# Kernel optimization log

Measured on AMD Instinct MI355X. Metric: run time of the kernel, lower is better.

## Reference

```python
import jax, jax.numpy as jnp
import numpy as np

B, L, D = 16, 2048, 192  # batch, frames_per_data, units
H, K = 4, 12             # num_heads, key_dim (hardcoded in build())
EPS = 1e-3               # keras LayerNormalization default epsilon


def layer_norm(x, g, b):
    m = jnp.mean(x, axis=-1, keepdims=True)
    v = jnp.mean(jnp.square(x - m), axis=-1, keepdims=True)
    return (x - m) * jax.lax.rsqrt(v + EPS) * g + b


def conv1d_valid(x, w, b):
    # x: [B,L,C], w: [3,Cin,Cout] -> [B,L-2,Cout]
    return jax.lax.conv_general_dilated(
        x, w, window_strides=(1,), padding='VALID',
        dimension_numbers=('NWC', 'WIO', 'NWC')) + b


def setup_inputs() -> dict:
    key = jax.random.key(0)
    ks = jax.random.split(key, 16)
    s = 0.05
    return {
        'x': jax.random.normal(ks[0], (B, L, D), jnp.float32),
        'ln1_g': jnp.ones((D,), jnp.float32),
        'ln1_b': jnp.zeros((D,), jnp.float32),
        'wq': jax.random.normal(ks[1], (D, H, K), jnp.float32) * s,
        'bq': jnp.zeros((H, K), jnp.float32),
        'wk': jax.random.normal(ks[2], (D, H, K), jnp.float32) * s,
        'bk': jnp.zeros((H, K), jnp.float32),
        'wv': jax.random.normal(ks[3], (D, H, K), jnp.float32) * s,
        'bv': jnp.zeros((H, K), jnp.float32),
        'wo': jax.random.normal(ks[4], (H, K, D), jnp.float32) * s,
        'bo': jnp.zeros((D,), jnp.float32),
        'ln2_g': jnp.ones((D,), jnp.float32),
        'ln2_b': jnp.zeros((D,), jnp.float32),
        'c1_w': jax.random.normal(ks[5], (3, D, D), jnp.float32) * s,
        'c1_b': jnp.zeros((D,), jnp.float32),
        'c2_w': jax.random.normal(ks[6], (3, D, D), jnp.float32) * s,
        'c2_b': jnp.zeros((D,), jnp.float32),
    }


def reference(x, ln1_g, ln1_b, wq, bq, wk, bk, wv, bv, wo, bo,
              ln2_g, ln2_b, c1_w, c1_b, c2_w, c2_b):
    # --- LN1 + causal MHA + residual (dropout = identity at inference) ---
    xn = layer_norm(x, ln1_g, ln1_b)
    q = jnp.einsum('bld,dhk->blhk', xn, wq) + bq
    k = jnp.einsum('bld,dhk->blhk', xn, wk) + bk
    v = jnp.einsum('bld,dhk->blhk', xn, wv) + bv
    scores = jnp.einsum('blhk,bmhk->bhlm', q, k) / jnp.sqrt(jnp.float32(K))
    causal = jnp.tril(jnp.ones((L, L), jnp.float32))  # tril(True) mask
    scores = scores + (1.0 - causal) * (-1e9)          # keras additive mask
    attn = jax.nn.softmax(scores, axis=-1)
    ctx = jnp.einsum('bhlm,bmhk->blhk', attn, v)
    mha = jnp.einsum('blhk,hkd->bld', ctx, wo) + bo
    x = x + mha
    # --- LN2 + positionwise Conv1D feedforward + residual ---
    xn = layer_norm(x, ln2_g, ln2_b)
    h = jax.nn.relu(conv1d_valid(xn, c1_w, c1_b))      # [B,L-2,D]
    h = jnp.pad(h, ((0, 0), (1, 1), (0, 0)))           # ZeroPadding1D(1,1)
    h = conv1d_valid(h, c2_w, c2_b)                    # [B,L-2,D]
    h = jnp.pad(h, ((0, 0), (1, 1), (0, 0)))
    return x + h
```

## Files before the change

### kernel.cpp

```cpp
#include <hip/hip_runtime.h>
#include <hip/hip_bf16.h>

#define L_ 2048
#define D_ 192
#define HK_ 48
#define EPS_ 1e-3f
#define SCALE_ 0.28867513459481287f
#define LOG2E_ 1.4426950408889634f

typedef __hip_bfloat16 bf16;
typedef _Float16 f16;
typedef __fp16 hf16x2 __attribute__((ext_vector_type(2)));
typedef _Float16 f16x4 __attribute__((ext_vector_type(4)));
typedef __bf16 bf16x4 __attribute__((ext_vector_type(4)));
typedef __bf16 bf16x8 __attribute__((ext_vector_type(8)));
typedef float  f32x4  __attribute__((ext_vector_type(4)));

__device__ __forceinline__ float b2f(bf16 x) { return __bfloat162float(x); }
__device__ __forceinline__ bf16 f2b(float x) { return __float2bfloat16(x); }

__global__ __launch_bounds__(256) void k_prep_all(
    const float* __restrict__ c1w, const float* __restrict__ c2w,
    const float* __restrict__ wq, const float* __restrict__ wk, const float* __restrict__ wv,
    const float* __restrict__ bq, const float* __restrict__ bk, const float* __restrict__ bv,
    const float* __restrict__ wo,
    bf16* __restrict__ wrep1, bf16* __restrict__ wrep2,
    bf16* __restrict__ wrepq, float* __restrict__ bias144, bf16* __restrict__ wrepo)
{
    const int i = blockIdx.x * 256 + threadIdx.x;
    if (i < 110592) {
        const int k = i / 192, n = i - k * 192;
        wrep1[((size_t)(k >> 5) * 192 + n) * 32 + (k & 31)] = f2b(c1w[i]);
    } else if (i < 221184) {
        const int j = i - 110592;
        const int k = j / 192, n = j - k * 192;
        wrep2[((size_t)(k >> 5) * 192 + n) * 32 + (k & 31)] = f2b(c2w[j]);
    } else if (i < 248832) {
        const int j = i - 221184;
        const int kb = j / 4608, rem = j % 4608;
        const int n = rem / 32, kk = rem % 32;
        const int k = kb * 32 + kk;
        float v;
        if (n < 48)       v = wq[k * HK_ + n] * (SCALE_ * LOG2E_);
        else if (n < 96)  v = wk[k * HK_ + (n - 48)];
        else              v = wv[k * HK_ + (n - 96)];
        wrepq[j] = f2b(v);
    } else if (i < 248976) {
        const int j = i - 248832;
        bias144[j] = (j < 48) ? bq[j] * (SCALE_ * LOG2E_)
                   : (j < 96) ? bk[j - 48] : bv[j - 96];
    } else if (i < 261264) {
        const int j = i - 248976;
        const int kb = j / 6144, rem = j % 6144;
        const int n = rem / 32, kk = rem % 32;
        const int k = kb * 32 + kk;
        wrepo[j] = f2b(k < 48 ? wo[k * D_ + n] : 0.f);
    }
}

__global__ __launch_bounds__(256, 4) void k_ln_qkv(
    const float* __restrict__ x, const float* __restrict__ g1, const float* __restrict__ b1,
    const bf16* __restrict__ wrep, const float* __restrict__ bias144,
    f16* __restrict__ qo, f16* __restrict__ ko, f16* __restrict__ vt)
{
    __shared__ bf16 xn[32 * 200];
    const int tid = threadIdx.x;
    const int wave = tid >> 6, lane = tid & 63;
    const int rowbase = blockIdx.x * 32;
    const int b = rowbase >> 11;
    const int lrow0 = rowbase & 2047;

    const float gg0 = g1[lane], gg1 = g1[lane + 64], gg2 = g1[lane + 128];
    const float bb0 = b1[lane], bb1 = b1[lane + 64], bb2 = b1[lane + 128];
    for (int i = 0; i < 8; ++i) {
        const int r = wave * 8 + i;
        const float* xp = x + (size_t)(rowbase + r) * D_;
        const float x0 = xp[lane];
        const float x1 = xp[lane + 64];
        const float x2 = xp[lane + 128];
        float s = x0 + x1 + x2;
        float q = x0 * x0 + x1 * x1 + x2 * x2;
        #pragma unroll
        for (int m = 1; m < 64; m <<= 1) {
            s += __shfl_xor(s, m, 64);
            q += __shfl_xor(q, m, 64);
        }
        const float mean = s * (1.0f / 192.0f);
        const float var  = q * (1.0f / 192.0f) - mean * mean;
        const float rs   = rsqrtf(var + EPS_);
        xn[r * 200 + lane]       = f2b((x0 - mean) * rs * gg0 + bb0);
        xn[r * 200 + lane + 64]  = f2b((x1 - mean) * rs * gg1 + bb1);
        xn[r * 200 + lane + 128] = f2b((x2 - mean) * rs * gg2 + bb2);
    }

    if (tid < 128) {
        const int h  = tid >> 5;
        const int vc = 12 + ((tid >> 3) & 3);
        const int p0 = lrow0 + (tid & 7) * 4;
        f16x4 vv;
        vv[0] = vv[1] = vv[2] = vv[3] = (vc == 12) ? (f16)1.0f : (f16)0.0f;
        *(f16x4*)(vt + ((size_t)(b * 4 + h) * 16 + vc) * 2048 + p0) = vv;
    }
    __syncthreads();

    const int l15 = lane & 15, q4 = lane >> 4;
    const int rt = wave >> 1, g = wave & 1;
    const int ntlim = 5 - g;
    f32x4 acc[5];
    #pragma unroll
    for (int nt = 0; nt < 5; ++nt) acc[nt] = (f32x4){0.f, 0.f, 0.f, 0.f};

    const bf16* xrow = xn + (rt * 16 + l15) * 200 + q4 * 8;
    #pragma unroll
    for (int kb = 0; kb < 6; ++kb) {
        const bf16x8 a = *(const bf16x8*)(xrow + kb * 32);
        const bf16* wp = wrep + ((size_t)kb * 144 + l15) * 32 + q4 * 8
                       + (size_t)(g * 5) * 16 * 32;
        #pragma unroll
        for (int nt = 0; nt < 5; ++nt) {
            if (nt < ntlim) {
                const bf16x8 bfr = *(const bf16x8*)(wp + (size_t)nt * 16 * 32);
                acc[nt] = __builtin_amdgcn_mfma_f32_16x16x32_bf16(a, bfr, acc[nt], 0, 0, 0);
            }
        }
    }

    const int lr0 = lrow0 + rt * 16 + q4 * 4;
    #pragma unroll
    for (int nt = 0; nt < 5; ++nt) {
        if (nt < ntlim) {
            const int ntg = g * 5 + nt;
            const int col = ntg * 16 + l15;
            const float bd = bias144[col];
            if (ntg < 3) {
                const int h2 = col / 12, c12 = col - h2 * 12;
                #pragma unroll
                for (int reg = 0; reg < 4; ++reg)
                    qo[((size_t)(b * 4 + h2) * 2048 + lr0 + reg) * 12 + c12] =
                        (f16)(acc[nt][reg] + bd);
            } else if (ntg < 6) {
                const int ck = col - 48;
                const int h2 = ck / 12, c12 = ck - h2 * 12;
                #pragma unroll
                for (int reg = 0; reg < 4; ++reg)
                    ko[((size_t)(b * 4 + h2) * 2048 + lr0 + reg) * 12 + c12] =
                        (f16)(acc[nt][reg] + bd);
            } else {
                const int vcol = col - 96;
                const int h = vcol / 12, c12 = vcol % 12;
                f16x4 vv;
                #pragma unroll
                for (int reg = 0; reg < 4; ++reg) vv[reg] = (f16)(acc[nt][reg] + bd);
                *(f16x4*)(vt + ((size_t)(b * 4 + h) * 16 + c12) * 2048 +
                          lrow0 + rt * 16 + q4 * 4) = vv;
            }
        }
    }
}

__global__ __launch_bounds__(256, 8) void k_attn(
    const f16* __restrict__ qh, const f16* __restrict__ kh, const f16* __restrict__ vt,
    bf16* __restrict__ ctx)
{
    const int tid = threadIdx.x;
    const int wv = tid >> 6, lane = tid & 63;
    const int quad = lane >> 4, l15 = lane & 15;
    const int bh = blockIdx.x & 63;
    const int qtile = 15 - (blockIdx.x >> 6);
    const int b = bh >> 2, h = bh & 3;
    const size_t base  = (size_t)bh * 2048 * 12;
    const size_t vbase = ((size_t)bh * 16 + l15) * 2048;
    const int qw = qtile * 128 + wv * 32;
    const int q16 = qw >> 4;
    const int ntot = q16 + 2;

    f16x4 Qf[2];
    #pragma unroll
    for (int s = 0; s < 2; ++s) {
        f16x4 v;
        if (quad < 3)
            v = *(const f16x4*)(qh + base + (size_t)(qw + s * 16 + l15) * 12 + quad * 4);
        else { v[0] = (f16)LOG2E_; v[1] = 0; v[2] = 0; v[3] = 0; }
        Qf[s] = v;
    }

    f32x4 O[2];
    O[0] = (f32x4){0.f, 0.f, 0.f, 0.f};
    O[1] = (f32x4){0.f, 0.f, 0.f, 0.f};

    f16x4 Kg[2], Vg[2];
    #pragma unroll
    for (int u = 0; u < 2; ++u) {
        if (quad < 3)
            Kg[u] = *(const f16x4*)(kh + base + (size_t)(u * 16 + l15) * 12 + quad * 4);
        else { Kg[u][0] = (f16)-6.0f; Kg[u][1] = 0; Kg[u][2] = 0; Kg[u][3] = 0; }
        Vg[u] = *(const f16x4*)(vt + vbase + u * 16 + quad * 4);
    }

    for (int t = 0; t < ntot; t += 2) {
        f16x4 Kn[2], Vn[2];
        if (t + 2 < ntot) {
            #pragma unroll
            for (int u = 0; u < 2; ++u) {
                const int kt = t + 2 + u;
                if (quad < 3)
                    Kn[u] = *(const f16x4*)(kh + base + (size_t)(kt * 16 + l15) * 12 + quad * 4);
                else { Kn[u][0] = (f16)-6.0f; Kn[u][1] = 0; Kn[u][2] = 0; Kn[u][3] = 0; }
                Vn[u] = *(const f16x4*)(vt + vbase + kt * 16 + quad * 4);
            }
        }
        const bool masked = (t >= q16);
        #pragma unroll
        for (int u = 0; u < 2; ++u) {
            const int k0 = (t + u) * 16 + quad * 4;
            #pragma unroll
            for (int s = 0; s < 2; ++s) {
                f32x4 sc = (f32x4){0.f, 0.f, 0.f, 0.f};
                sc = __builtin_amdgcn_mfma_f32_16x16x16f16(Kg[u], Qf[s], sc, 0, 0, 0);
                float p0 = __builtin_amdgcn_exp2f(sc[0]);
                float p1 = __builtin_amdgcn_exp2f(sc[1]);
                float p2 = __builtin_amdgcn_exp2f(sc[2]);
                float p3 = __builtin_amdgcn_exp2f(sc[3]);
                if (masked) {
                    const int qg = qw + s * 16 + l15;
                    p0 = (k0 + 0 <= qg) ? p0 : 0.f;
                    p1 = (k0 + 1 <= qg) ? p1 : 0.f;
                    p2 = (k0 + 2 <= qg) ? p2 : 0.f;
                    p3 = (k0 + 3 <= qg) ? p3 : 0.f;
                }
                const hf16x2 lo = __builtin_amdgcn_cvt_pkrtz(p0, p1);
                const hf16x2 hi = __builtin_amdgcn_cvt_pkrtz(p2, p3);
                f16x4 p;
                p[0] = (f16)lo[0]; p[1] = (f16)lo[1];
                p[2] = (f16)hi[0]; p[3] = (f16)hi[1];
                O[s] = __builtin_amdgcn_mfma_f32_16x16x16f16(p, Vg[u], O[s], 0, 0, 0);
            }
        }
        Kg[0] = Kn[0]; Kg[1] = Kn[1];
        Vg[0] = Vn[0]; Vg[1] = Vn[1];
    }

    const int src = (quad << 4) + 12;
    #pragma unroll
    for (int s = 0; s < 2; ++s) {
        #pragma unroll
        for (int j = 0; j < 4; ++j) {
            const float li  = __shfl(O[s][j], src, 64);
            const float inv = __builtin_amdgcn_rcpf(li);
            if (l15 < 12)
                ctx[(size_t)(b * 2048 + qw + s * 16 + quad * 4 + j) * 48 + h * 12 + l15]
                    = f2b(O[s][j] * inv);
        }
    }
}

__global__ __launch_bounds__(256, 4) void k_proj_ln2(
    const float* __restrict__ x, const bf16* __restrict__ ctx,
    const bf16* __restrict__ wrepo,
    const float* __restrict__ bo, const float* __restrict__ g2,
    const float* __restrict__ lb2, bf16* __restrict__ x2b,
    bf16* __restrict__ xn2b)
{
    __shared__ bf16 ct[32 * 72];
    __shared__ float psum[4][4][4][2];
    const int tid = threadIdx.x;
    const int wave = tid >> 6, lane = tid & 63;
    const int rowbase = blockIdx.x * 32;

    {
        const int row6 = tid / 6, c6 = tid - row6 * 6;
        if (tid < 192) {
            const bf16x8 v = *(const bf16x8*)(ctx + (size_t)(rowbase + row6) * 48 + c6 * 8);
            *(bf16x8*)(ct + row6 * 72 + c6 * 8) = v;
        }
        const int rz = tid / 3, cz = tid - rz * 3;
        if (tid < 96) {
            bf16x8 z;
            #pragma unroll
            for (int i = 0; i < 8; ++i) z[i] = (__bf16)0.0f;
            *(bf16x8*)(ct + rz * 72 + 48 + cz * 8) = z;
        }
    }
    __syncthreads();

    const int l15 = lane & 15, q4 = lane >> 4;
    const int rt = wave >> 1, g = wave & 1;
    f32x4 acc[6];
    #pragma unroll
    for (int j = 0; j < 6; ++j) acc[j] = (f32x4){0.f, 0.f, 0.f, 0.f};
    const bf16* arow = ct + (rt * 16 + l15) * 72 + q4 * 8;
    #pragma unroll
    for (int kb = 0; kb < 2; ++kb) {
        const bf16x8 a = *(const bf16x8*)(arow + kb * 32);
        const bf16* wp = wrepo + ((size_t)kb * 192 + l15) * 32 + q4 * 8
                       + (size_t)(g * 6) * 16 * 32;
        #pragma unroll
        for (int j = 0; j < 6; ++j) {
            const bf16x8 bb = *(const bf16x8*)(wp + (size_t)j * 16 * 32);
            acc[j] = __builtin_amdgcn_mfma_f32_16x16x32_bf16(a, bb, acc[j], 0, 0, 0);
        }
    }

    const int rw0 = rowbase + rt * 16 + q4 * 4;
    float sum[4] = {0.f, 0.f, 0.f, 0.f}, ssum[4] = {0.f, 0.f, 0.f, 0.f};
    #pragma unroll
    for (int j = 0; j < 6; ++j) {
        const int col = (g * 6 + j) * 16 + l15;
        const float bod = bo[col];
        #pragma unroll
        for (int reg = 0; reg < 4; ++reg) {
            const float v = acc[j][reg] + bod + x[(size_t)(rw0 + reg) * D_ + col];
            acc[j][reg] = v;
            x2b[(size_t)(rw0 + reg) * D_ + col] = f2b(v);
            sum[reg] += v; ssum[reg] += v * v;
        }
    }
    #pragma unroll
    for (int m = 1; m <= 8; m <<= 1) {
        #pragma unroll
        for (int reg = 0; reg < 4; ++reg) {
            sum[reg]  += __shfl_xor(sum[reg], m, 64);
            ssum[reg] += __shfl_xor(ssum[reg], m, 64);
        }
    }
    if (l15 == 0) {
        #pragma unroll
        for (int reg = 0; reg < 4; ++reg) {
            psum[wave][q4][reg][0] = sum[reg];
            psum[wave][q4][reg][1] = ssum[reg];
        }
    }
    __syncthreads();
    float mean[4], rs[4];
    #pragma unroll
    for (int reg = 0; reg < 4; ++reg) {
        const float st  = sum[reg]  + psum[wave ^ 1][q4][reg][0];
        const float qt2 = ssum[reg] + psum[wave ^ 1][q4][reg][1];
        mean[reg] = st * (1.0f / 192.0f);
        const float var = qt2 * (1.0f / 192.0f) - mean[reg] * mean[reg];
        rs[reg] = rsqrtf(var + EPS_);
    }
    #pragma unroll
    for (int j = 0; j < 6; ++j) {
        const int col = (g * 6 + j) * 16 + l15;
        const float gg = g2[col], bb2 = lb2[col];
        #pragma unroll
        for (int reg = 0; reg < 4; ++reg)
            xn2b[(size_t)(rw0 + reg) * D_ + col] =
                f2b((acc[j][reg] - mean[reg]) * rs[reg] * gg + bb2);
    }
}

#define INROWB 416
#define NIN    36
#define NH     34
#define HTOFF  (NIN * INROWB)
__global__ __launch_bounds__(256, 4) void k_conv_fused(
    const bf16* __restrict__ act, const bf16* __restrict__ w1,
    const float* __restrict__ b1c, const bf16* __restrict__ w2,
    const float* __restrict__ b2c, const bf16* __restrict__ x2b,
    float* __restrict__ outf)
{
    __shared__ __align__(16) char lds[NIN * INROWB + NH * INROWB];

    const int tid = threadIdx.x;
    const int wave = tid >> 6, lane = tid & 63;
    const int m16 = lane & 15, q = lane >> 4;
    const int rowbase = blockIdx.x * 32;
    const int lrow = rowbase & (L_ - 1);

    {
        const bf16* src0 = act + ((long long)rowbase - 2) * D_;
        bf16x8 v[4];
        int dst[4];
        #pragma unroll
        for (int i = 0; i < 4; ++i) {
            const int g = tid + i * 256;
            if (g < 864) {
                v[i] = *(const bf16x8*)(src0 + g * 8);
                const int row = (g * 2731) >> 16;
                dst[i] = row * INROWB + (g - row * 24) * 16;
            }
        }
        #pragma unroll
        for (int i = 0; i < 4; ++i) {
            const int g = tid + i * 256;
            if (g < 864) *(bf16x8*)(lds + dst[i]) = v[i];
        }
    }

    const int laneA = m16 * INROWB + q * 16;
    const int colw = wave * 48;
    float bd1[3], bd2[3];
    #pragma unroll
    for (int j = 0; j < 3; ++j) {
        bd1[j] = b1c[colw + j * 16 + m16];
        bd2[j] = b2c[colw + j * 16 + m16];
    }
    __syncthreads();

    f32x4 acc1[3][3];
    #pragma unroll
    for (int mt = 0; mt < 3; ++mt)
        #pragma unroll
        for (int j = 0; j < 3; ++j) acc1[mt][j] = (f32x4){0.f, 0.f, 0.f, 0.f};

    #define LOADB(w, kb, j) \
        (*(const bf16x8*)((w) + ((size_t)(kb) * 192 + m16) * 32 + q * 8 \
                          + (size_t)(wave * 3 + (j)) * 16 * 32))
    {
        bf16x8 bB[2][3];
        #pragma unroll
        for (int j = 0; j < 3; ++j) bB[0][j] = LOADB(w1, 0, j);
        #pragma unroll
        for (int kb = 0; kb < 18; ++kb) {
            if (kb + 1 < 18) {
                #pragma unroll
                for (int j = 0; j < 3; ++j) bB[(kb + 1) & 1][j] = LOADB(w1, kb + 1, j);
            }
            const int t = kb / 6, c6 = kb % 6;
            bf16x8 a[3];
            #pragma unroll
            for (int mt = 0; mt < 3; ++mt)
                a[mt] = *(const bf16x8*)(lds + laneA + (mt * 16 + t) * INROWB + c6 * 64);
            #pragma unroll
            for (int j = 0; j < 3; ++j)
                #pragma unroll
                for (int mt = 0; mt < 3; ++mt)
                    acc1[mt][j] = __builtin_amdgcn_mfma_f32_16x16x32_bf16(
                        a[mt], bB[kb & 1][j], acc1[mt][j], 0, 0, 0);
        }
    }

    #pragma unroll
    for (int mt = 0; mt < 3; ++mt)
        #pragma unroll
        for (int j = 0; j < 3; ++j)
            #pragma unroll
            for (int reg = 0; reg < 4; ++reg) {
                const int hr = mt * 16 + q * 4 + reg;
                if (hr < NH) {
                    const int hm = lrow + hr - 1;
                    float v = fmaxf(acc1[mt][j][reg] + bd1[j], 0.f);
                    if (hm == 0 || hm == L_ - 1) v = 0.f;
                    *(bf16*)(lds + HTOFF + hr * INROWB + (colw + j * 16 + m16) * 2) = f2b(v);
                }
            }

    float xr[3][2][4];
    #pragma unroll
    for (int j = 0; j < 3; ++j)
        #pragma unroll
        for (int mt = 0; mt < 2; ++mt)
            #pragma unroll
            for (int reg = 0; reg < 4; ++reg)
                xr[j][mt][reg] = b2f(x2b[(size_t)(rowbase + mt * 16 + q * 4 + reg) * D_
                                         + colw + j * 16 + m16]);
    __syncthreads();

    f32x4 acc2[2][3];
    #pragma unroll
    for (int mt = 0; mt < 2; ++mt)
        #pragma unroll
        for (int j = 0; j < 3; ++j) acc2[mt][j] = (f32x4){0.f, 0.f, 0.f, 0.f};
    {
        bf16x8 bB[2][3];
        #pragma unroll
        for (int j = 0; j < 3; ++j) bB[0][j] = LOADB(w2, 0, j);
        #pragma unroll
        for (int kb = 0; kb < 18; ++kb) {
            if (kb + 1 < 18) {
                #pragma unroll
                for (int j = 0; j < 3; ++j) bB[(kb + 1) & 1][j] = LOADB(w2, kb + 1, j);
            }
            const int t = kb / 6, c6 = kb % 6;
            bf16x8 a[2];
            #pragma unroll
            for (int mt = 0; mt < 2; ++mt)
                a[mt] = *(const bf16x8*)(lds + HTOFF + laneA + (mt * 16 + t) * INROWB + c6 * 64);
            #pragma unroll
            for (int j = 0; j < 3; ++j)
                #pragma unroll
                for (int mt = 0; mt < 2; ++mt)
                    acc2[mt][j] = __builtin_amdgcn_mfma_f32_16x16x32_bf16(
                        a[mt], bB[kb & 1][j], acc2[mt][j], 0, 0, 0);
        }
    }
    #undef LOADB

    #pragma unroll
    for (int j = 0; j < 3; ++j)
        #pragma unroll
        for (int mt = 0; mt < 2; ++mt)
            #pragma unroll
            for (int reg = 0; reg < 4; ++reg) {
                const int r = rowbase + mt * 16 + q * 4 + reg;
                const int m = r & (L_ - 1);
                float v = xr[j][mt][reg];
                if (m != 0 && m != L_ - 1) v += acc2[mt][j][reg] + bd2[j];
                outf[(size_t)r * D_ + colw + j * 16 + m16] = v;
            }
}

extern "C" void kernel_launch(void* const* d_in, const int* in_sizes, int n_in,
                              void* d_out, int out_size, void* d_ws, size_t ws_size,
                              hipStream_t stream)
{
    const float* x    = (const float*)d_in[0];
    const float* ln1g = (const float*)d_in[1];
    const float* ln1b = (const float*)d_in[2];
    const float* wq   = (const float*)d_in[3];
    const float* bq   = (const float*)d_in[4];
    const float* wk   = (const float*)d_in[5];
    const float* bk   = (const float*)d_in[6];
    const float* wv   = (const float*)d_in[7];
    const float* bv   = (const float*)d_in[8];
    const float* wo   = (const float*)d_in[9];
    const float* bo   = (const float*)d_in[10];
    const float* ln2g = (const float*)d_in[11];
    const float* ln2b = (const float*)d_in[12];
    const float* c1w  = (const float*)d_in[13];
    const float* c1b  = (const float*)d_in[14];
    const float* c2w  = (const float*)d_in[15];
    const float* c2b  = (const float*)d_in[16];

    const size_t ROWS = (size_t)16 * L_;
    char* ws = (char*)d_ws;
    size_t off = 4096;
    bf16* xn2b = (bf16*)(ws + off); off += ROWS * D_ * 2;
    off += 4096;
    bf16* hpb  = (bf16*)(ws + off); off += ROWS * D_ * 2;
    off += 4096;
    bf16* x2b  = (bf16*)(ws + off); off += ROWS * D_ * 2;
    f16* qb    = (f16*)(ws + off);   off += ROWS * HK_ * 2;
    f16* kb    = (f16*)(ws + off);   off += ROWS * HK_ * 2;
    f16* vt    = (f16*)(ws + off);   off += (size_t)64 * 16 * 2048 * 2;
    bf16* ctx  = (bf16*)(ws + off);  off += ROWS * 48 * 2;
    bf16* wrep1 = (bf16*)(ws + off); off += 576 * 192 * 2;
    bf16* wrep2 = (bf16*)(ws + off); off += 576 * 192 * 2;
    bf16* wrepq = (bf16*)(ws + off); off += 6 * 144 * 32 * 2;
    float* bias144 = (float*)(ws + off); off += 144 * 4;
    bf16* wrepo = (bf16*)(ws + off); off += 2 * 192 * 32 * 2;

    (void)hpb;
    k_prep_all   <<<1021, 256, 0, stream>>>(c1w, c2w, wq, wk, wv, bq, bk, bv, wo,
                                            wrep1, wrep2, wrepq, bias144, wrepo);
    k_ln_qkv     <<<1024, 256, 0, stream>>>(x, ln1g, ln1b, wrepq, bias144, qb, kb, vt);
    k_attn       <<<1024, 256, 0, stream>>>(qb, kb, vt, ctx);
    k_proj_ln2   <<<1024, 256, 0, stream>>>(x, ctx, wrepo, bo, ln2g, ln2b,
                                            x2b, xn2b);
    k_conv_fused <<<1024, 256, 0, stream>>>(xn2b, wrep1, c1b, wrep2, c2b, x2b,
                                            (float*)d_out);
}
```

Measured before the change: 219.8 us.

## Split attention into 16-row query strips per wave with double-buffered K/V groups

Each wave in the attention kernel now handles one 16-row query tile instead of two, and the grid doubles to 2048 blocks of 64-query strips. This gives finer causal load balancing and more parallelism. K/V fragments are loaded in groups of four key tiles with ping-pong register buffers to hide load latency. The causal mask is now applied on every tile rather than only the diagonal ones. The trade-offs are that K/V loads are no longer shared across two query tiles per wave, and the register footprint for buffering grows.

```diff
diff --git a/kernel.cpp b/kernel.cpp
--- a/kernel.cpp
+++ b/kernel.cpp
@@ -166,91 +166,76 @@
     const int wv = tid >> 6, lane = tid & 63;
     const int quad = lane >> 4, l15 = lane & 15;
     const int bh = blockIdx.x & 63;
-    const int qtile = 15 - (blockIdx.x >> 6);
+    const int strip = 31 - (blockIdx.x >> 6);
     const int b = bh >> 2, h = bh & 3;
     const size_t base  = (size_t)bh * 2048 * 12;
     const size_t vbase = ((size_t)bh * 16 + l15) * 2048;
-    const int qw = qtile * 128 + wv * 32;
-    const int q16 = qw >> 4;
-    const int ntot = q16 + 2;
-
-    f16x4 Qf[2];
-    #pragma unroll
-    for (int s = 0; s < 2; ++s) {
-        f16x4 v;
-        if (quad < 3)
-            v = *(const f16x4*)(qh + base + (size_t)(qw + s * 16 + l15) * 12 + quad * 4);
-        else { v[0] = (f16)LOG2E_; v[1] = 0; v[2] = 0; v[3] = 0; }
-        Qf[s] = v;
-    }
-
-    f32x4 O[2];
-    O[0] = (f32x4){0.f, 0.f, 0.f, 0.f};
-    O[1] = (f32x4){0.f, 0.f, 0.f, 0.f};
-
-    f16x4 Kg[2], Vg[2];
-    #pragma unroll
-    for (int u = 0; u < 2; ++u) {
-        if (quad < 3)
-            Kg[u] = *(const f16x4*)(kh + base + (size_t)(u * 16 + l15) * 12 + quad * 4);
-        else { Kg[u][0] = (f16)-6.0f; Kg[u][1] = 0; Kg[u][2] = 0; Kg[u][3] = 0; }
-        Vg[u] = *(const f16x4*)(vt + vbase + u * 16 + quad * 4);
-    }
-
-    for (int t = 0; t < ntot; t += 2) {
-        f16x4 Kn[2], Vn[2];
-        if (t + 2 < ntot) {
-            #pragma unroll
-            for (int u = 0; u < 2; ++u) {
-                const int kt = t + 2 + u;
-                if (quad < 3)
-                    Kn[u] = *(const f16x4*)(kh + base + (size_t)(kt * 16 + l15) * 12 + quad * 4);
-                else { Kn[u][0] = (f16)-6.0f; Kn[u][1] = 0; Kn[u][2] = 0; Kn[u][3] = 0; }
-                Vn[u] = *(const f16x4*)(vt + vbase + kt * 16 + quad * 4);
-            }
-        }
-        const bool masked = (t >= q16);
-        #pragma unroll
-        for (int u = 0; u < 2; ++u) {
-            const int k0 = (t + u) * 16 + quad * 4;
-            #pragma unroll
-            for (int s = 0; s < 2; ++s) {
-                f32x4 sc = (f32x4){0.f, 0.f, 0.f, 0.f};
-                sc = __builtin_amdgcn_mfma_f32_16x16x16f16(Kg[u], Qf[s], sc, 0, 0, 0);
-                float p0 = __builtin_amdgcn_exp2f(sc[0]);
-                float p1 = __builtin_amdgcn_exp2f(sc[1]);
-                float p2 = __builtin_amdgcn_exp2f(sc[2]);
-                float p3 = __builtin_amdgcn_exp2f(sc[3]);
-                if (masked) {
-                    const int qg = qw + s * 16 + l15;
-                    p0 = (k0 + 0 <= qg) ? p0 : 0.f;
-                    p1 = (k0 + 1 <= qg) ? p1 : 0.f;
-                    p2 = (k0 + 2 <= qg) ? p2 : 0.f;
-                    p3 = (k0 + 3 <= qg) ? p3 : 0.f;
-                }
-                const hf16x2 lo = __builtin_amdgcn_cvt_pkrtz(p0, p1);
-                const hf16x2 hi = __builtin_amdgcn_cvt_pkrtz(p2, p3);
-                f16x4 p;
-                p[0] = (f16)lo[0]; p[1] = (f16)lo[1];
-                p[2] = (f16)hi[0]; p[3] = (f16)hi[1];
-                O[s] = __builtin_amdgcn_mfma_f32_16x16x16f16(p, Vg[u], O[s], 0, 0, 0);
-            }
-        }
-        Kg[0] = Kn[0]; Kg[1] = Kn[1];
-        Vg[0] = Vn[0]; Vg[1] = Vn[1];
+    const int qw = strip * 64 + wv * 16;
+    const int qg = qw + l15;
+    const int ngroups = strip + 1;
+
+    f16x4 Qf;
+    if (quad < 3)
+        Qf = *(const f16x4*)(qh + base + (size_t)(qw + l15) * 12 + quad * 4);
+    else { Qf[0] = (f16)LOG2E_; Qf[1] = 0; Qf[2] = 0; Qf[3] = 0; }
+
+    f32x4 O = (f32x4){0.f, 0.f, 0.f, 0.f};
+
+    f16x4 KA[4], VA[4], KB[4], VB[4];
+
+    auto LOADG = [&](f16x4* K, f16x4* V, int g) {
+        const int t0 = g * 4;
+        #pragma unroll
+        for (int u = 0; u < 4; ++u) {
+            if (quad < 3)
+                K[u] = *(const f16x4*)(kh + base + (size_t)((t0 + u) * 16 + l15) * 12 + quad * 4);
+            else { K[u][0] = (f16)-6.0f; K[u][1] = 0; K[u][2] = 0; K[u][3] = 0; }
+            V[u] = *(const f16x4*)(vt + vbase + (t0 + u) * 16 + quad * 4);
+        }
+    };
+    auto COMPUTE = [&](const f16x4* K, const f16x4* V, int g) {
+        const int t0 = g * 4;
+        #pragma unroll
+        for (int u = 0; u < 4; ++u) {
+            f32x4 sc = (f32x4){0.f, 0.f, 0.f, 0.f};
+            sc = __builtin_amdgcn_mfma_f32_16x16x16f16(K[u], Qf, sc, 0, 0, 0);
+            const int k0 = (t0 + u) * 16 + quad * 4;
+            float p0 = __builtin_amdgcn_exp2f(sc[0]);
+            float p1 = __builtin_amdgcn_exp2f(sc[1]);
+            float p2 = __builtin_amdgcn_exp2f(sc[2]);
+            float p3 = __builtin_amdgcn_exp2f(sc[3]);
+            p0 = (k0 + 0 <= qg) ? p0 : 0.f;
+            p1 = (k0 + 1 <= qg) ? p1 : 0.f;
+            p2 = (k0 + 2 <= qg) ? p2 : 0.f;
+            p3 = (k0 + 3 <= qg) ? p3 : 0.f;
+            const hf16x2 lo = __builtin_amdgcn_cvt_pkrtz(p0, p1);
+            const hf16x2 hi = __builtin_amdgcn_cvt_pkrtz(p2, p3);
+            f16x4 p;
+            p[0] = (f16)lo[0]; p[1] = (f16)lo[1];
+            p[2] = (f16)hi[0]; p[3] = (f16)hi[1];
+            O = __builtin_amdgcn_mfma_f32_16x16x16f16(p, V[u], O, 0, 0, 0);
+        }
+    };
+
+    LOADG(KA, VA, 0);
+    int g = 0;
+    while (true) {
+        if (g + 1 < ngroups) LOADG(KB, VB, g + 1);
+        COMPUTE(KA, VA, g);
+        ++g; if (g >= ngroups) break;
+        if (g + 1 < ngroups) LOADG(KA, VA, g + 1);
+        COMPUTE(KB, VB, g);
+        ++g; if (g >= ngroups) break;
     }
 
     const int src = (quad << 4) + 12;
     #pragma unroll
-    for (int s = 0; s < 2; ++s) {
-        #pragma unroll
-        for (int j = 0; j < 4; ++j) {
-            const float li  = __shfl(O[s][j], src, 64);
-            const float inv = __builtin_amdgcn_rcpf(li);
-            if (l15 < 12)
-                ctx[(size_t)(b * 2048 + qw + s * 16 + quad * 4 + j) * 48 + h * 12 + l15]
-                    = f2b(O[s][j] * inv);
-        }
+    for (int j = 0; j < 4; ++j) {
+        const float li  = __shfl(O[j], src, 64);
+        const float inv = __builtin_amdgcn_rcpf(li);
+        if (l15 < 12)
+            ctx[(size_t)(b * 2048 + qw + quad * 4 + j) * 48 + h * 12 + l15]
+                = f2b(O[j] * inv);
     }
 }
 
@@ -546,7 +531,7 @@
     k_prep_all   <<<1021, 256, 0, stream>>>(c1w, c2w, wq, wk, wv, bq, bk, bv, wo,
                                             wrep1, wrep2, wrepq, bias144, wrepo);
     k_ln_qkv     <<<1024, 256, 0, stream>>>(x, ln1g, ln1b, wrepq, bias144, qb, kb, vt);
-    k_attn       <<<1024, 256, 0, stream>>>(qb, kb, vt, ctx);
+    k_attn       <<<2048, 256, 0, stream>>>(qb, kb, vt, ctx);
     k_proj_ln2   <<<1024, 256, 0, stream>>>(x, ctx, wrepo, bo, ln2g, ln2b,
                                             x2b, xn2b);
     k_conv_fused <<<1024, 256, 0, stream>>>(xn2b, wrep1, c1b, wrep2, c2b, x2b,
```

Result: slower. 241.7 us (+10.0%).
